# Kernel tuning notes

Hardware: AMD Instinct MI355X
Metric: run time of the kernel (lower is better)

Reference implementation:

```python
import jax, jax.numpy as jnp
import numpy as np
import math

EMBED_DIM = 1024
NUM_HEADS = 16
B, S = 4, 4096
NEG_INF = -1e30


def setup_inputs() -> dict:
    key = jax.random.key(0)
    k1, k2, k3, k4 = jax.random.split(key, 4)
    D = EMBED_DIM
    # xavier_uniform bounds
    lim_in = math.sqrt(6.0 / (3 * D + D))
    lim_out = math.sqrt(6.0 / (D + D))
    return {
        "x": jax.random.normal(k1, (B, S, D), dtype=jnp.float32),
        "in_proj_weight": jax.random.uniform(k2, (3 * D, D), dtype=jnp.float32, minval=-lim_in, maxval=lim_in),
        "in_proj_bias": jnp.zeros((3 * D,), dtype=jnp.float32),
        "out_proj_weight": jax.random.uniform(k3, (D, D), dtype=jnp.float32, minval=-lim_out, maxval=lim_out),
        "out_proj_bias": jnp.zeros((D,), dtype=jnp.float32),
    }


def _cron_root_attention(q, k, v):
    """Causal sqrt(N) block-sparse attention.

    q,k,v: [B, H, S, hd]. Sequence split into nb blocks of size b = sqrt(S).
    Each query attends to: (a) keys in its own block (causal within block),
    (b) one summary key per strictly-previous block (the block's last key).
    Complexity O(S * (b + nb)) = O(N * sqrt(N)).
    """
    Bq, H, Sq, hd = q.shape
    b = int(round(math.sqrt(Sq)))
    nb = Sq // b
    scale = 1.0 / math.sqrt(hd)

    qb = q.reshape(Bq, H, nb, b, hd)
    kb = k.reshape(Bq, H, nb, b, hd)
    vb = v.reshape(Bq, H, nb, b, hd)
    ks = k[:, :, b - 1::b, :]  # [B, H, nb, hd] summary keys (last of each block)
    vs = v[:, :, b - 1::b, :]

    # local (within-block) scores, causal mask
    s_loc = jnp.einsum("bhnqd,bhnkd->bhnqk", qb, kb) * scale  # [B,H,nb,b,b]
    idx = jnp.arange(b)
    loc_mask = idx[:, None] >= idx[None, :]  # [b, b]
    s_loc = jnp.where(loc_mask[None, None, None], s_loc, NEG_INF)

    # strided scores to summary keys of strictly previous blocks
    s_str = jnp.einsum("bhnqd,bhmd->bhnqm", qb, ks) * scale  # [B,H,nb,b,nb]
    nidx = jnp.arange(nb)
    str_mask = nidx[:, None] > nidx[None, :]  # [nb(query block), nb(key block)]
    s_str = jnp.where(str_mask[None, None, :, None, :], s_str, NEG_INF)

    # joint softmax over local + strided keys
    scores = jnp.concatenate([s_loc, s_str], axis=-1)  # [B,H,nb,b,b+nb]
    w = jax.nn.softmax(scores, axis=-1)
    w_loc, w_str = w[..., :b], w[..., b:]

    out = jnp.einsum("bhnqk,bhnkd->bhnqd", w_loc, vb) \
        + jnp.einsum("bhnqm,bhmd->bhnqd", w_str, vs)
    return out.reshape(Bq, H, Sq, hd)


def reference(x, in_proj_weight, in_proj_bias, out_proj_weight, out_proj_bias):
    Bx, Sx, D = x.shape
    H = NUM_HEADS
    hd = D // H
    qkv = x @ in_proj_weight.T + in_proj_bias  # [B,S,3D]
    qkv = jnp.transpose(qkv.reshape(Bx, Sx, 3, H, hd), (2, 0, 3, 1, 4))
    q, k, v = qkv[0], qkv[1], qkv[2]  # each [B,H,S,hd]
    out = _cron_root_attention(q, k, v)  # [B,H,S,hd]
    out = jnp.transpose(out, (0, 2, 1, 3)).reshape(Bx, Sx, D)
    return out @ out_proj_weight.T + out_proj_bias
```

## Files before the change

### kernel.cpp

```cpp
#include <hip/hip_runtime.h>
#include <stdint.h>

typedef __attribute__((ext_vector_type(8))) short short8;
typedef __attribute__((ext_vector_type(4))) float f32x4;
typedef __attribute__((ext_vector_type(4))) float f4;
typedef __attribute__((ext_vector_type(4))) ushort us4;

#define AS1 __attribute__((address_space(1)))
#define AS3 __attribute__((address_space(3)))

__device__ __forceinline__ ushort f2bf(float f) {
  uint u = __builtin_bit_cast(uint, f);
  u += 0x7fffu + ((u >> 16) & 1u);
  return (ushort)(u >> 16);
}

__global__ void cvt_all(const float* __restrict__ x, const float* __restrict__ wi,
                        const float* __restrict__ wo, ushort* __restrict__ xb,
                        ushort* __restrict__ wib, ushort* __restrict__ wob) {
  const int n_x = (16384 * 1024) / 4;
  const int n_wi = (3072 * 1024) / 4;
  const int n_wo = (1024 * 1024) / 4;
  const int n_tot = n_x + n_wi + n_wo;
  int i = blockIdx.x * blockDim.x + threadIdx.x;
  int stride = gridDim.x * blockDim.x;
  for (; i < n_tot; i += stride) {
    const float* src;
    ushort* dst;
    int idx;
    if (i < n_x) {
      src = x; dst = xb; idx = i;
    } else if (i < n_x + n_wi) {
      src = wi; dst = wib; idx = i - n_x;
    } else {
      src = wo; dst = wob; idx = i - n_x - n_wi;
    }
    f4 v = ((const f4*)src)[idx];
    us4 o;
    o[0] = f2bf(v[0]); o[1] = f2bf(v[1]); o[2] = f2bf(v[2]); o[3] = f2bf(v[3]);
    ((us4*)dst)[idx] = o;
  }
}


__device__ __forceinline__ void stage_half(const ushort* __restrict__ g, int pitch,
                                           int row0, int k0, char* ldsbase, int tid) {
#pragma unroll
  for (int i = 0; i < 2; ++i) {
    uint chunk = i * 512 + tid;
    uint Q = chunk << 4;
    uint L = Q ^ (((Q >> 7) & 7u) << 4);
    uint row = L >> 7;
    uint kb = L & 127u;
    const char* gp = (const char*)(g + (size_t)(row0 + (int)row) * pitch + k0) + kb;
    char* lp = ldsbase + ((i * 512 + (tid & ~63)) << 4);
    __builtin_amdgcn_global_load_lds((const AS1 void*)gp, (AS3 void*)lp, 16, 0, 0);
  }
}

__device__ __forceinline__ void stage_j(int j, const ushort* __restrict__ A,
                                        const ushort* __restrict__ Bw, int K,
                                        int arow0, int brow0, char* sA, char* sB, int tid) {
  int t = j >> 2, h = j & 3;
  int k0 = t << 6;
  char* base = ((h < 2) ? sB : sA) + ((t & 1) << 15) + ((h & 1) << 14);
  const ushort* g = (h < 2) ? Bw : A;
  int row0 = ((h < 2) ? brow0 : arow0) + ((h & 1) << 7);
  stage_half(g, K, row0, k0, base, tid);
}

template <int OUT_F32>
__global__ __launch_bounds__(512, 1) void gemm256(const ushort* __restrict__ A,
                                                  const ushort* __restrict__ Bw,
                                                  const float* __restrict__ bias,
                                                  void* __restrict__ Cout,
                                                  int M, int N, int K, int gm) {
  __shared__ char sA[65536];
  __shared__ char sB[65536];
  const int tid = threadIdx.x;
  const int lane = tid & 63, l15 = lane & 15, lk = lane >> 4;
  const int w = tid >> 6;
  const int wm = w >> 2, wn = w & 3;
  const int NT = K >> 6;

  int q8 = gridDim.x >> 3;
  int bid = blockIdx.x;
  int swz = (bid & 7) * q8 + (bid >> 3);
  int bm = swz % gm, bn = swz / gm;
  const int arow0 = bm << 8, brow0 = bn << 8;

  f32x4 acc[8][4];
  f32x4 zero = {0.f, 0.f, 0.f, 0.f};
#pragma unroll
  for (int i = 0; i < 8; ++i)
#pragma unroll
    for (int j = 0; j < 4; ++j) acc[i][j] = zero;

#pragma unroll
  for (int j = 0; j < 7; ++j) stage_j(j, A, Bw, K, arow0, brow0, sA, sB, tid);
  asm volatile("s_waitcnt vmcnt(6)" ::: "memory");
  __builtin_amdgcn_s_barrier();

  for (int t = 0; t < NT; ++t) {
    const char* bA = sA + ((t & 1) << 15);
    const char* bB = sB + ((t & 1) << 15);
    short8 bfr[4][2];
#pragma unroll
    for (int qd = 0; qd < 4; ++qd) {
      short8 afr[2][2];
      if (qd == 0) {
#pragma unroll
        for (int ni = 0; ni < 4; ++ni)
#pragma unroll
          for (int kk = 0; kk < 2; ++kk) {
            uint row = (uint)(wn * 64 + ni * 16 + l15);
            uint byte = (row << 7) + (kk << 6) + (lk << 4);
            bfr[ni][kk] = *(const short8*)&bB[byte ^ ((row & 7u) << 4)];
          }
      }
#pragma unroll
      for (int mi = 0; mi < 2; ++mi)
#pragma unroll
        for (int kk = 0; kk < 2; ++kk) {
          uint row = (uint)(wm * 128 + (qd * 2 + mi) * 16 + l15);
          uint byte = (row << 7) + (kk << 6) + (lk << 4);
          afr[mi][kk] = *(const short8*)&bA[byte ^ ((row & 7u) << 4)];
        }
      int j = 4 * t + qd + 7;
      if (j < 4 * NT) stage_j(j, A, Bw, K, arow0, brow0, sA, sB, tid);
      if (qd == 3) {
        if (t < NT - 2) asm volatile("s_waitcnt vmcnt(6)" ::: "memory");
        else if (t == NT - 2) asm volatile("s_waitcnt vmcnt(0)" ::: "memory");
      }
      __builtin_amdgcn_s_barrier();
      asm volatile("s_waitcnt lgkmcnt(0)" ::: "memory");
      __builtin_amdgcn_s_setprio(1);
#pragma unroll
      for (int kk = 0; kk < 2; ++kk)
#pragma unroll
        for (int mi = 0; mi < 2; ++mi)
#pragma unroll
          for (int ni = 0; ni < 4; ++ni)
            acc[qd * 2 + mi][ni] = __builtin_amdgcn_mfma_f32_16x16x32_bf16(
                afr[mi][kk], bfr[ni][kk], acc[qd * 2 + mi][ni], 0, 0, 0);
      __builtin_amdgcn_s_setprio(0);
      __builtin_amdgcn_s_barrier();
    }
  }

#pragma unroll
  for (int m = 0; m < 8; ++m)
#pragma unroll
    for (int ni = 0; ni < 4; ++ni)
#pragma unroll
      for (int r = 0; r < 4; ++r) {
        int row = arow0 + wm * 128 + m * 16 + lk * 4 + r;
        int col = brow0 + wn * 64 + ni * 16 + l15;
        float v = acc[m][ni][r] + bias[col];
        if constexpr (OUT_F32)
          ((float*)Cout)[(size_t)row * N + col] = v;
        else
          ((ushort*)Cout)[(size_t)row * N + col] = f2bf(v);
      }
}

__global__ __launch_bounds__(256) void cron_attn(const ushort* __restrict__ qkv,
                                                 ushort* __restrict__ aout) {
  const int S = 4096, CQ = 3072;
  int bid = blockIdx.x;
  int n = bid & 63;
  int h = (bid >> 6) & 15;
  int b = bid >> 10;
  int tid = threadIdx.x;
  int w = tid >> 6, lane = tid & 63, l15 = lane & 15, lk = lane >> 4;

  const ushort* qp = qkv + (size_t)b * S * CQ + h * 64;
  const ushort* kp = qp + 1024;
  const ushort* vp = qp + 2048;

  __shared__ char vT[16384];
  __shared__ char pL[4][4096];

  {
    int r = tid >> 1;
    int half = tid & 1;
    int srow = (r < 64) ? (n * 64 + r) : ((r - 64) * 64 + 63);
    const ushort* src = vp + (size_t)srow * CQ + half * 32;
    short8 vv0 = ((const short8*)src)[0];
    short8 vv1 = ((const short8*)src)[1];
    short8 vv2 = ((const short8*)src)[2];
    short8 vv3 = ((const short8*)src)[3];
#pragma unroll
    for (int j = 0; j < 8; ++j) {
      int d0 = half * 32 + j;
      *(short*)&vT[(uint)(d0 * 256 + r * 2) ^ (((uint)d0 & 7u) << 4)] = vv0[j];
      int d1 = half * 32 + 8 + j;
      *(short*)&vT[(uint)(d1 * 256 + r * 2) ^ (((uint)d1 & 7u) << 4)] = vv1[j];
      int d2 = half * 32 + 16 + j;
      *(short*)&vT[(uint)(d2 * 256 + r * 2) ^ (((uint)d2 & 7u) << 4)] = vv2[j];
      int d3 = half * 32 + 24 + j;
      *(short*)&vT[(uint)(d3 * 256 + r * 2) ^ (((uint)d3 & 7u) << 4)] = vv3[j];
    }
  }
  __syncthreads();

  short8 aq[2];
  {
    int srow = n * 64 + w * 16 + l15;
#pragma unroll
    for (int kk = 0; kk < 2; ++kk)
      aq[kk] = *(const short8*)(qp + (size_t)srow * CQ + kk * 32 + lk * 8);
  }

  f32x4 sc[8];
  f32x4 zero = {0.f, 0.f, 0.f, 0.f};
#pragma unroll
  for (int c = 0; c < 8; ++c) sc[c] = zero;
#pragma unroll
  for (int c = 0; c < 8; ++c) {
    int key = (c < 4) ? (n * 64 + c * 16 + l15) : (((c - 4) * 16 + l15) * 64 + 63);
    const ushort* kr = kp + (size_t)key * CQ;
#pragma unroll
    for (int kk = 0; kk < 2; ++kk) {
      short8 bk = *(const short8*)(kr + kk * 32 + lk * 8);
      sc[c] = __builtin_amdgcn_mfma_f32_16x16x32_bf16(aq[kk], bk, sc[c], 0, 0, 0);
    }
  }

  float p[8][4];
  int qrow = w * 16 + lk * 4;
#pragma unroll
  for (int c = 0; c < 8; ++c)
#pragma unroll
    for (int r = 0; r < 4; ++r) {
      float s = sc[c][r] * 0.125f;
      bool ok = (c < 4) ? ((qrow + r) >= (c * 16 + l15)) : (((c - 4) * 16 + l15) < n);
      p[c][r] = ok ? s : -1e30f;
    }

#pragma unroll
  for (int r = 0; r < 4; ++r) {
    float m = p[0][r];
#pragma unroll
    for (int c = 1; c < 8; ++c) m = fmaxf(m, p[c][r]);
    m = fmaxf(m, __shfl_xor(m, 1));
    m = fmaxf(m, __shfl_xor(m, 2));
    m = fmaxf(m, __shfl_xor(m, 4));
    m = fmaxf(m, __shfl_xor(m, 8));
    float sum = 0.f;
#pragma unroll
    for (int c = 0; c < 8; ++c) {
      p[c][r] = __expf(p[c][r] - m);
      sum += p[c][r];
    }
    sum += __shfl_xor(sum, 1);
    sum += __shfl_xor(sum, 2);
    sum += __shfl_xor(sum, 4);
    sum += __shfl_xor(sum, 8);
    float rs = 1.f / sum;
#pragma unroll
    for (int c = 0; c < 8; ++c) p[c][r] *= rs;
  }

  char* myP = pL[w];
#pragma unroll
  for (int c = 0; c < 8; ++c)
#pragma unroll
    for (int r = 0; r < 4; ++r) {
      uint row = lk * 4 + r;
      uint byte = row * 256 + (c * 16 + l15) * 2;
      *(short*)&myP[byte ^ ((row & 7u) << 4)] = (short)f2bf(p[c][r]);
    }
  short8 ap[4];
#pragma unroll
  for (int kk = 0; kk < 4; ++kk) {
    uint row = (uint)l15;
    uint byte = row * 256 + (kk * 32 + lk * 8) * 2;
    ap[kk] = *(const short8*)&myP[byte ^ ((row & 7u) << 4)];
  }

  f32x4 ao[4];
#pragma unroll
  for (int dc = 0; dc < 4; ++dc) ao[dc] = zero;
#pragma unroll
  for (int dc = 0; dc < 4; ++dc)
#pragma unroll
    for (int kk = 0; kk < 4; ++kk) {
      uint d = dc * 16 + l15;
      uint byte = d * 256 + (kk * 32 + lk * 8) * 2;
      short8 bv = *(const short8*)&vT[byte ^ ((d & 7u) << 4)];
      ao[dc] = __builtin_amdgcn_mfma_f32_16x16x32_bf16(ap[kk], bv, ao[dc], 0, 0, 0);
    }

#pragma unroll
  for (int dc = 0; dc < 4; ++dc)
#pragma unroll
    for (int r = 0; r < 4; ++r) {
      int srow = n * 64 + w * 16 + lk * 4 + r;
      int col = h * 64 + dc * 16 + l15;
      aout[((size_t)(b * S + srow)) * 1024 + col] = f2bf(ao[dc][r]);
    }
}

extern "C" void kernel_launch(void* const* d_in, const int* in_sizes, int n_in,
                              void* d_out, int out_size, void* d_ws, size_t ws_size,
                              hipStream_t stream) {
  const float* x = (const float*)d_in[0];
  const float* wi = (const float*)d_in[1];
  const float* bi = (const float*)d_in[2];
  const float* wo = (const float*)d_in[3];
  const float* bo = (const float*)d_in[4];
  float* out = (float*)d_out;
  char* ws = (char*)d_ws;

  ushort* xb = (ushort*)(ws);
  ushort* wib = (ushort*)(ws + (size_t)33554432);
  ushort* wob = (ushort*)(ws + (size_t)39845888);
  ushort* qkvb = (ushort*)(ws + (size_t)41943040);
  ushort* aob = (ushort*)(ws + (size_t)142606336);

  cvt_all<<<2048, 256, 0, stream>>>(x, wi, wo, xb, wib, wob);

  gemm256<0><<<64 * 12, 512, 0, stream>>>(xb, wib, bi, qkvb, 16384, 3072, 1024, 64);
  cron_attn<<<4096, 256, 0, stream>>>(qkvb, aob);
  gemm256<1><<<64 * 4, 512, 0, stream>>>(aob, wob, bo, out, 16384, 1024, 1024, 64);
}
```

Baseline: 226.3 us.

## Make QKV GEMM persistent over multiple tiles with cross-tile prefetch

The QKV projection GEMM is now a persistent kernel. Each of 256 workgroups processes 3 consecutive output tiles, and K-chunk staging runs continuously across tile boundaries, so the next tile's loads overlap the current tile's MFMA work and epilogue. This targets wave quantization (768 tiles on 256 CUs) and the pipeline drain and refill cost at each tile start. In exchange, K is hardcoded to 1024, the tile order changes to row-major (bm = T/GN) and alters L2 locality, and the epilogue stores now sit inside the main loop.

```diff
diff --git a/kernel.cpp b/kernel.cpp
--- a/kernel.cpp
+++ b/kernel.cpp
@@ -43,7 +43,7 @@
 }
 
 
-__device__ __forceinline__ void stage_half(const ushort* __restrict__ g, int pitch,
+__device__ __forceinline__ void stage_half(const ushort* __restrict__ g,
                                            int row0, int k0, char* ldsbase, int tid) {
 #pragma unroll
   for (int i = 0; i < 2; ++i) {
@@ -52,42 +52,45 @@
     uint L = Q ^ (((Q >> 7) & 7u) << 4);
     uint row = L >> 7;
     uint kb = L & 127u;
-    const char* gp = (const char*)(g + (size_t)(row0 + (int)row) * pitch + k0) + kb;
+    const char* gp = (const char*)(g + (size_t)(row0 + (int)row) * 1024 + k0) + kb;
     char* lp = ldsbase + ((i * 512 + (tid & ~63)) << 4);
     __builtin_amdgcn_global_load_lds((const AS1 void*)gp, (AS3 void*)lp, 16, 0, 0);
   }
 }
 
-__device__ __forceinline__ void stage_j(int j, const ushort* __restrict__ A,
-                                        const ushort* __restrict__ Bw, int K,
-                                        int arow0, int brow0, char* sA, char* sB, int tid) {
-  int t = j >> 2, h = j & 3;
+template <int GN>
+__device__ __forceinline__ void stage_g(int j, int Tbase, const ushort* __restrict__ A,
+                                        const ushort* __restrict__ Bw,
+                                        char* sA, char* sB, int tid) {
+  int tile = j >> 6;
+  int jj = j & 63;
+  int t = jj >> 2, h = jj & 3;
+  int T = Tbase + tile;
+  int bm = T / GN, bn = T % GN;
   int k0 = t << 6;
-  char* base = ((h < 2) ? sB : sA) + ((t & 1) << 15) + ((h & 1) << 14);
+  char* base = ((h < 2) ? sB : sA) + ((((uint)j >> 2) & 1u) << 15) + ((h & 1) << 14);
   const ushort* g = (h < 2) ? Bw : A;
-  int row0 = ((h < 2) ? brow0 : arow0) + ((h & 1) << 7);
-  stage_half(g, K, row0, k0, base, tid);
-}
-
-template <int OUT_F32>
-__global__ __launch_bounds__(512, 1) void gemm256(const ushort* __restrict__ A,
-                                                  const ushort* __restrict__ Bw,
-                                                  const float* __restrict__ bias,
-                                                  void* __restrict__ Cout,
-                                                  int M, int N, int K, int gm) {
+  int row0 = (((h < 2) ? bn : bm) << 8) + ((h & 1) << 7);
+  stage_half(g, row0, k0, base, tid);
+}
+
+template <int OUT_F32, int GN, int NTILE>
+__global__ __launch_bounds__(512, 1) void gemm256p(const ushort* __restrict__ A,
+                                                   const ushort* __restrict__ Bw,
+                                                   const float* __restrict__ bias,
+                                                   void* __restrict__ Cout, int N) {
   __shared__ char sA[65536];
   __shared__ char sB[65536];
   const int tid = threadIdx.x;
   const int lane = tid & 63, l15 = lane & 15, lk = lane >> 4;
   const int w = tid >> 6;
   const int wm = w >> 2, wn = w & 3;
-  const int NT = K >> 6;
+  const int TOT = 16 * NTILE;
 
   int q8 = gridDim.x >> 3;
-  int bid = blockIdx.x;
-  int swz = (bid & 7) * q8 + (bid >> 3);
-  int bm = swz % gm, bn = swz / gm;
-  const int arow0 = bm << 8, brow0 = bn << 8;
+  int g = blockIdx.x;
+  int gs = (g & 7) * q8 + (g >> 3);
+  const int Tbase = gs * NTILE;
 
   f32x4 acc[8][4];
   f32x4 zero = {0.f, 0.f, 0.f, 0.f};
@@ -97,13 +100,14 @@
     for (int j = 0; j < 4; ++j) acc[i][j] = zero;
 
 #pragma unroll
-  for (int j = 0; j < 7; ++j) stage_j(j, A, Bw, K, arow0, brow0, sA, sB, tid);
+  for (int j = 0; j < 7; ++j) stage_g<GN>(j, Tbase, A, Bw, sA, sB, tid);
   asm volatile("s_waitcnt vmcnt(6)" ::: "memory");
   __builtin_amdgcn_s_barrier();
 
-  for (int t = 0; t < NT; ++t) {
-    const char* bA = sA + ((t & 1) << 15);
-    const char* bB = sB + ((t & 1) << 15);
+#pragma unroll 1
+  for (int tg = 0; tg < TOT; ++tg) {
+    const char* bA = sA + ((tg & 1) << 15);
+    const char* bB = sB + ((tg & 1) << 15);
     short8 bfr[4][2];
 #pragma unroll
     for (int qd = 0; qd < 4; ++qd) {
@@ -126,11 +130,11 @@
           uint byte = (row << 7) + (kk << 6) + (lk << 4);
           afr[mi][kk] = *(const short8*)&bA[byte ^ ((row & 7u) << 4)];
         }
-      int j = 4 * t + qd + 7;
-      if (j < 4 * NT) stage_j(j, A, Bw, K, arow0, brow0, sA, sB, tid);
+      int j = 4 * tg + qd + 7;
+      if (j < 4 * TOT) stage_g<GN>(j, Tbase, A, Bw, sA, sB, tid);
       if (qd == 3) {
-        if (t < NT - 2) asm volatile("s_waitcnt vmcnt(6)" ::: "memory");
-        else if (t == NT - 2) asm volatile("s_waitcnt vmcnt(0)" ::: "memory");
+        if (tg < TOT - 2) asm volatile("s_waitcnt vmcnt(6)" ::: "memory");
+        else if (tg == TOT - 2) asm volatile("s_waitcnt vmcnt(0)" ::: "memory");
       }
       __builtin_amdgcn_s_barrier();
       asm volatile("s_waitcnt lgkmcnt(0)" ::: "memory");
@@ -146,22 +150,30 @@
       __builtin_amdgcn_s_setprio(0);
       __builtin_amdgcn_s_barrier();
     }
-  }
-
-#pragma unroll
-  for (int m = 0; m < 8; ++m)
-#pragma unroll
-    for (int ni = 0; ni < 4; ++ni)
-#pragma unroll
-      for (int r = 0; r < 4; ++r) {
-        int row = arow0 + wm * 128 + m * 16 + lk * 4 + r;
-        int col = brow0 + wn * 64 + ni * 16 + l15;
-        float v = acc[m][ni][r] + bias[col];
-        if constexpr (OUT_F32)
-          ((float*)Cout)[(size_t)row * N + col] = v;
-        else
-          ((ushort*)Cout)[(size_t)row * N + col] = f2bf(v);
-      }
+
+    if ((tg & 15) == 15) {
+      int T = Tbase + (tg >> 4);
+      int arow0 = (T / GN) << 8, brow0 = (T % GN) << 8;
+#pragma unroll
+      for (int m = 0; m < 8; ++m)
+#pragma unroll
+        for (int ni = 0; ni < 4; ++ni)
+#pragma unroll
+          for (int r = 0; r < 4; ++r) {
+            int row = arow0 + wm * 128 + m * 16 + lk * 4 + r;
+            int col = brow0 + wn * 64 + ni * 16 + l15;
+            float v = acc[m][ni][r] + bias[col];
+            if constexpr (OUT_F32)
+              ((float*)Cout)[(size_t)row * N + col] = v;
+            else
+              ((ushort*)Cout)[(size_t)row * N + col] = f2bf(v);
+          }
+#pragma unroll
+      for (int i = 0; i < 8; ++i)
+#pragma unroll
+        for (int jz = 0; jz < 4; ++jz) acc[i][jz] = zero;
+    }
+  }
 }
 
 __global__ __launch_bounds__(256) void cron_attn(const ushort* __restrict__ qkv,
@@ -321,7 +333,7 @@
 
   cvt_all<<<2048, 256, 0, stream>>>(x, wi, wo, xb, wib, wob);
 
-  gemm256<0><<<64 * 12, 512, 0, stream>>>(xb, wib, bi, qkvb, 16384, 3072, 1024, 64);
+  gemm256p<0, 12, 3><<<256, 512, 0, stream>>>(xb, wib, bi, qkvb, 3072);
   cron_attn<<<4096, 256, 0, stream>>>(qkvb, aob);
-  gemm256<1><<<64 * 4, 512, 0, stream>>>(aob, wob, bo, out, 16384, 1024, 1024, 64);
-}
+  gemm256p<1, 4, 1><<<256, 512, 0, stream>>>(aob, wob, bo, out, 1024);
+}
```

Result: slower. 262.2 us (+15.9%).
